# Performance work log

Hardware: AMD Instinct MI355X
Metric: run time of the kernel (lower is better)

Reference implementation:

```python
import jax, jax.numpy as jnp
import numpy as np

KERNEL = 3
PAD = (KERNEL - 1) // 2  # 'same' padding applied manually, conv itself is VALID


def _conv2d(x, w, padding):
    # x: (N,H,W,Cin), w: (kh,kw,Cin,Cout)
    return jax.lax.conv_general_dilated(
        x, w, window_strides=(1, 1), padding=padding,
        dimension_numbers=('NHWC', 'HWIO', 'NHWC'))


def convlstm2d(x, kernel, rec_kernel, bias):
    """Keras ConvLSTM2D (valid input conv on pre-padded input, SAME recurrent conv).

    x: (B,T,H,W,Cin); kernel: (k,k,Cin,4F); rec_kernel: (k,k,F,4F); bias: (4F,)
    Returns full hidden sequence (B,T,H,W,F).
    """
    # tf.pad with paddings [[0,0],[0,0],[p,p],[p,p],[0,0]] (constant mode)
    xp = jnp.pad(x, ((0, 0), (0, 0), (PAD, PAD), (PAD, PAD), (0, 0)))
    B, T = x.shape[:2]
    # Fuse the input-to-hidden conv across all timesteps in one big conv
    xz = _conv2d(xp.reshape((B * T,) + xp.shape[2:]), kernel, 'VALID') + bias
    H, W, F4 = xz.shape[1:]
    F = F4 // 4
    xz = xz.reshape(B, T, H, W, F4).transpose(1, 0, 2, 3, 4)  # (T,B,H,W,4F)

    def step(carry, xt):
        h, c = carry
        z = xt + _conv2d(h, rec_kernel, 'SAME')
        zi, zf, zc, zo = jnp.split(z, 4, axis=-1)  # Keras gate order i,f,c,o
        i = jax.nn.sigmoid(zi)
        f = jax.nn.sigmoid(zf)
        c = f * c + i * jnp.tanh(zc)
        o = jax.nn.sigmoid(zo)
        h = o * jnp.tanh(c)
        return (h, c), h

    h0 = jnp.zeros((B, H, W, F), x.dtype)
    (_, _), hs = jax.lax.scan(step, (h0, h0), xz)
    return hs.transpose(1, 0, 2, 3, 4)  # (B,T,H,W,F)


def setup_inputs() -> dict:
    key = jax.random.key(0)
    ks = jax.random.split(key, 7)
    B, T, H, W, Cin, F = 4, 16, 64, 64, 32, 32
    std = float(np.sqrt(2.0 / (KERNEL * KERNEL * F)))  # he-style kernel init
    x = jax.random.normal(ks[0], (B, T, H, W, Cin), jnp.float32)
    k1 = jax.random.normal(ks[1], (KERNEL, KERNEL, Cin, 4 * F), jnp.float32) * std
    rk1 = jax.random.normal(ks[2], (KERNEL, KERNEL, F, 4 * F), jnp.float32) * std
    b1 = jnp.zeros((4 * F,), jnp.float32)
    k2 = jax.random.normal(ks[3], (KERNEL, KERNEL, F, 4 * F), jnp.float32) * std
    rk2 = jax.random.normal(ks[4], (KERNEL, KERNEL, F, 4 * F), jnp.float32) * std
    b2 = jnp.zeros((4 * F,), jnp.float32)
    return {"x": x, "k1": k1, "rk1": rk1, "b1": b1, "k2": k2, "rk2": rk2, "b2": b2}


def reference(x, k1, rk1, b1, k2, rk2, b2):
    # normalization=None -> identity; pad + ConvLSTM2D, twice
    h = convlstm2d(x, k1, rk1, b1)
    h = convlstm2d(h, k2, rk2, b2)
    return h
```

## Files before the change

kernel.cpp:

```cpp
#include <hip/hip_runtime.h>


typedef __bf16 bf16x8 __attribute__((ext_vector_type(8)));
typedef float f32x4 __attribute__((ext_vector_type(4)));

#define WPK_ELEMS 73728
#define PLANE 524288

__device__ __forceinline__ float fsigmoid(float z) {
    return 1.0f / (1.0f + __expf(-z));
}
__device__ __forceinline__ float ftanh(float z) {
    z = fminf(15.0f, fmaxf(-15.0f, z));
    float e = __expf(2.0f * z);
    return (e - 1.0f) / (e + 1.0f);
}

__global__ __launch_bounds__(256) void pack_weights(
    const float* __restrict__ wk1, const float* __restrict__ wr1,
    const float* __restrict__ wk2, const float* __restrict__ wr2,
    __bf16* __restrict__ wpk)
{
    int i = blockIdx.x * 256 + threadIdx.x;
    if (i >= 2 * WPK_ELEMS) return;
    int layer = i / WPK_ELEMS;
    int r = i - layer * WPK_ELEMS;
    int j2 = r & 7;
    int L  = (r >> 3) & 63;
    int nt = (r >> 9) & 7;
    int cix = r >> 12;
    int tap = cix >> 1, src = cix & 1;
    int s = ((L >> 4) << 3) + j2;
    int gate = nt & 3;
    int f = ((nt >> 2) << 4) + (L & 15);
    int n = (gate << 5) + f;
    const float* w = layer ? (src ? wr2 : wk2) : (src ? wr1 : wk1);
    wpk[i] = (__bf16)w[(tap * 32 + s) * 128 + n];
}

__device__ __forceinline__ bf16x8 cvt8(const float* p) {
    const float4 f0 = *(const float4*)p;
    const float4 f1 = *(const float4*)(p + 4);
    bf16x8 v;
    v[0] = (__bf16)f0.x; v[1] = (__bf16)f0.y;
    v[2] = (__bf16)f0.z; v[3] = (__bf16)f0.w;
    v[4] = (__bf16)f1.x; v[5] = (__bf16)f1.y;
    v[6] = (__bf16)f1.z; v[7] = (__bf16)f1.w;
    return v;
}

#define MFMA8(A0, A1, WP)                                                              \
    acc[0][0] = __builtin_amdgcn_mfma_f32_16x16x32_bf16(A0, WP[0],   acc[0][0], 0, 0, 0); \
    acc[0][1] = __builtin_amdgcn_mfma_f32_16x16x32_bf16(A0, WP[64],  acc[0][1], 0, 0, 0); \
    acc[0][2] = __builtin_amdgcn_mfma_f32_16x16x32_bf16(A0, WP[128], acc[0][2], 0, 0, 0); \
    acc[0][3] = __builtin_amdgcn_mfma_f32_16x16x32_bf16(A0, WP[192], acc[0][3], 0, 0, 0); \
    acc[1][0] = __builtin_amdgcn_mfma_f32_16x16x32_bf16(A1, WP[0],   acc[1][0], 0, 0, 0); \
    acc[1][1] = __builtin_amdgcn_mfma_f32_16x16x32_bf16(A1, WP[64],  acc[1][1], 0, 0, 0); \
    acc[1][2] = __builtin_amdgcn_mfma_f32_16x16x32_bf16(A1, WP[128], acc[1][2], 0, 0, 0); \
    acc[1][3] = __builtin_amdgcn_mfma_f32_16x16x32_bf16(A1, WP[192], acc[1][3], 0, 0, 0);

#define MFMA4(A0, WP)                                                                  \
    acc1[0] = __builtin_amdgcn_mfma_f32_16x16x32_bf16(A0, WP[0],   acc1[0], 0, 0, 0);     \
    acc1[1] = __builtin_amdgcn_mfma_f32_16x16x32_bf16(A0, WP[64],  acc1[1], 0, 0, 0);     \
    acc1[2] = __builtin_amdgcn_mfma_f32_16x16x32_bf16(A0, WP[128], acc1[2], 0, 0, 0);     \
    acc1[3] = __builtin_amdgcn_mfma_f32_16x16x32_bf16(A0, WP[192], acc1[3], 0, 0, 0);

__global__ __launch_bounds__(1024, 1) void clstm_pair3(
    const float* __restrict__ x,
    const __bf16* __restrict__ wpk1, const __bf16* __restrict__ wpk2,
    const float* __restrict__ bias1, const float* __restrict__ bias2,
    __bf16* __restrict__ h1buf,
    __bf16* __restrict__ h2buf,
    float* __restrict__ c1,
    float* __restrict__ c2,
    float* __restrict__ out, int j)
{
    __shared__ __bf16 tXA[6 * 66 * 36];
    __shared__ __bf16 tRA[6 * 66 * 36];
    __shared__ __bf16 tXB[4 * 66 * 36];
    __shared__ __bf16 tHA[4 * 66 * 36];
    __shared__ float  cpass[2 * 64 * 32];

    const int blk = blockIdx.x;
    const int k = blk >> 3;
    const int layer = k >> 4;
    if (layer ? (j < 1) : (j > 7)) return;
    const int grp = (blk & 7) * 16 + (k & 15);
    const int T0 = layer ? (2 * j - 2) : (2 * j);
    const int R = grp << 1;
    const int b = R >> 6, y0 = R & 63;

    const int tid = threadIdx.x;
    const int wid = tid >> 6, L = tid & 63;
    const int c = L & 15, q = L >> 4;

    const int wr  = wid >> 2;
    const int fhA = (wid >> 1) & 1;
    const int mpA = wid & 1;
    const int fA  = fhA * 16 + c;
    const int o   = wid >> 3;
    const int fhB = (wid >> 2) & 1;
    const int pxq = wid & 3;
    const int fB  = fhB * 16 + c;

    const bf16x8* wpkv = (const bf16x8*)(layer ? wpk2 : wpk1);
    const float* bias = layer ? bias2 : bias1;
    float bvA[4], bvB[4];
    #pragma unroll
    for (int g = 0; g < 4; ++g) {
        bvA[g] = bias[g * 32 + fA];
        bvB[g] = bias[g * 32 + fB];
    }

    const float*  xA  = x + (size_t)(b * 16 + T0) * 131072;
    const float*  xB  = xA + 131072;
    const __bf16* h1A = h1buf + (size_t)(T0 & 3) * PLANE;
    const __bf16* h1B = h1buf + (size_t)((T0 + 1) & 3) * PLANE;
    const __bf16* hRA = layer ? (h2buf + (size_t)(((T0 - 1) >> 1) & 1) * PLANE)
                              : (h1buf + (size_t)((T0 - 1) & 3) * PLANE);

    const int n1 = T0 ? 3168 : 1584;
    for (int i = tid; i < n1; i += 1024) {
        const int tile = (i >= 1584);
        const int r2 = i - tile * 1584;
        const int g = r2 & 3;
        const int rc = r2 >> 2;
        const int cc = rc % 66;
        const int row = rc / 66;
        const int yy = y0 - 2 + row;
        const int xc = cc - 1;
        bf16x8 v = {};
        if (yy >= 0 && yy < 64 && xc >= 0 && xc < 64) {
            if (!layer && !tile) {
                v = cvt8(xA + ((size_t)yy * 64 + xc) * 32 + g * 8);
            } else {
                const __bf16* s = tile ? hRA : h1A;
                v = *(const bf16x8*)(s + (((size_t)(b * 64 + yy)) * 64 + xc) * 32 + g * 8);
            }
        }
        *(bf16x8*)((tile ? tRA : tXA) + (row * 66 + cc) * 36 + g * 8) = v;
    }
    for (int i = tid; i < 1056; i += 1024) {
        const int g = i & 3;
        const int rc = i >> 2;
        const int cc = rc % 66;
        const int row = rc / 66;
        const int yy = y0 - 1 + row;
        const int xc = cc - 1;
        bf16x8 v = {};
        if (yy >= 0 && yy < 64 && xc >= 0 && xc < 64) {
            if (!layer) v = cvt8(xB + ((size_t)yy * 64 + xc) * 32 + g * 8);
            else        v = *(const bf16x8*)(h1B + (((size_t)(b * 64 + yy)) * 64 + xc) * 32 + g * 8);
        }
        *(bf16x8*)(tXB + (row * 66 + cc) * 36 + g * 8) = v;
    }
    for (int i = tid; i < 1188; i += 1024)
        *(bf16x8*)(tHA + i * 8) = (bf16x8){};
    __syncthreads();

    {
        const int ra = y0 - 1 + wr;
        const bool rvalid = (ra >= 0 && ra < 64);
        const bool own = (wr == 1 || wr == 2);
        const float* crd = (layer ? c2 : c1) + (size_t)(((T0 - 1) >> 1) & 1) * PLANE;
        const size_t rowA = (size_t)(b * 64 + (rvalid ? ra : 0)) * 2048;

        f32x4 acc[2][4];
        #pragma unroll
        for (int m2 = 0; m2 < 2; ++m2)
            #pragma unroll
            for (int g = 0; g < 4; ++g)
                acc[m2][g] = (f32x4){bvA[g], bvA[g], bvA[g], bvA[g]};

        #pragma unroll
        for (int tap = 0; tap < 9; ++tap) {
            const int dyk = tap / 3, dxk = tap % 3;
            const int lb = ((wr + dyk) * 66 + mpA * 32 + c + dxk) * 36 + q * 8;
            const bf16x8 a0 = *(const bf16x8*)(tXA + lb);
            const bf16x8 a1 = *(const bf16x8*)(tXA + lb + 16 * 36);
            const bf16x8* wpx = wpkv + (size_t)((tap * 2) * 8 + fhA * 4) * 64 + L;
            MFMA8(a0, a1, wpx);
            if (T0 > 0) {
                const bf16x8 h0 = *(const bf16x8*)(tRA + lb);
                const bf16x8 h1v = *(const bf16x8*)(tRA + lb + 16 * 36);
                const bf16x8* wph = wpkv + (size_t)((tap * 2 + 1) * 8 + fhA * 4) * 64 + L;
                MFMA8(h0, h1v, wph);
            }
        }
        #pragma unroll
        for (int m2 = 0; m2 < 2; ++m2) {
            #pragma unroll
            for (int r = 0; r < 4; ++r) {
                const int px = mpA * 32 + m2 * 16 + q * 4 + r;
                const float ig = fsigmoid(acc[m2][0][r]);
                const float fg = fsigmoid(acc[m2][1][r]);
                const float gg = ftanh(acc[m2][2][r]);
                const float og = fsigmoid(acc[m2][3][r]);
                float cold = 0.f;
                if (T0 > 0 && rvalid) cold = crd[rowA + (size_t)px * 32 + fA];
                const float cn = (T0 ? fg * cold : 0.f) + ig * gg;
                const float hv = og * ftanh(cn);
                if (rvalid) tHA[(wr * 66 + px + 1) * 36 + fA] = (__bf16)hv;
                if (own) {
                    cpass[(wr - 1) * 2048 + px * 32 + fA] = cn;
                    if (layer)
                        out[((size_t)(b * 16 + T0) * 4096 + (size_t)ra * 64 + px) * 32 + fA] = hv;
                    else
                        h1buf[(size_t)(T0 & 3) * PLANE + rowA + (size_t)px * 32 + fA] = (__bf16)hv;
                }
            }
        }
    }
    __syncthreads();

    {
        const int rb = y0 + o;
        float* cwr = (layer ? c2 : c1) + (size_t)(((T0 + 1) >> 1) & 1) * PLANE;

        f32x4 acc1[4];
        #pragma unroll
        for (int g = 0; g < 4; ++g)
            acc1[g] = (f32x4){bvB[g], bvB[g], bvB[g], bvB[g]};

        #pragma unroll
        for (int tap = 0; tap < 9; ++tap) {
            const int dyk = tap / 3, dxk = tap % 3;
            const int lb = ((o + dyk) * 66 + pxq * 16 + c + dxk) * 36 + q * 8;
            const bf16x8 a0 = *(const bf16x8*)(tXB + lb);
            const bf16x8* wpx = wpkv + (size_t)((tap * 2) * 8 + fhB * 4) * 64 + L;
            MFMA4(a0, wpx);
            const bf16x8 h0 = *(const bf16x8*)(tHA + lb);
            const bf16x8* wph = wpkv + (size_t)((tap * 2 + 1) * 8 + fhB * 4) * 64 + L;
            MFMA4(h0, wph);
        }
        const size_t rowB = (size_t)(b * 64 + rb) * 2048;
        __bf16* h2w = h2buf + (size_t)(((T0 + 1) >> 1) & 1) * PLANE;
        #pragma unroll
        for (int r = 0; r < 4; ++r) {
            const int px = pxq * 16 + q * 4 + r;
            const float ig = fsigmoid(acc1[0][r]);
            const float fg = fsigmoid(acc1[1][r]);
            const float gg = ftanh(acc1[2][r]);
            const float og = fsigmoid(acc1[3][r]);
            const float cold = cpass[o * 2048 + px * 32 + fB];
            const float cn = fg * cold + ig * gg;
            const float hv = og * ftanh(cn);
            cwr[rowB + (size_t)px * 32 + fB] = cn;
            if (layer) {
                out[((size_t)(b * 16 + T0 + 1) * 4096 + (size_t)rb * 64 + px) * 32 + fB] = hv;
                h2w[rowB + (size_t)px * 32 + fB] = (__bf16)hv;
            } else {
                h1buf[(size_t)((T0 + 1) & 3) * PLANE + rowB + (size_t)px * 32 + fB] = (__bf16)hv;
            }
        }
    }
}

extern "C" void kernel_launch(void* const* d_in, const int* in_sizes, int n_in,
                              void* d_out, int out_size, void* d_ws, size_t ws_size,
                              hipStream_t stream)
{
    const float* x   = (const float*)d_in[0];
    const float* k1  = (const float*)d_in[1];
    const float* rk1 = (const float*)d_in[2];
    const float* b1  = (const float*)d_in[3];
    const float* k2  = (const float*)d_in[4];
    const float* rk2 = (const float*)d_in[5];
    const float* b2  = (const float*)d_in[6];
    float* out = (float*)d_out;

    __bf16* wpk1  = (__bf16*)d_ws;
    __bf16* wpk2  = wpk1 + WPK_ELEMS;
    __bf16* h1buf = wpk2 + WPK_ELEMS;
    __bf16* h2buf = h1buf + 4 * (size_t)PLANE;
    float*  c1    = (float*)(h2buf + 2 * (size_t)PLANE);
    float*  c2    = c1 + 2 * (size_t)PLANE;

    pack_weights<<<(2 * WPK_ELEMS + 255) / 256, 256, 0, stream>>>(k1, rk1, k2, rk2, wpk1);

    for (int j = 0; j <= 8; ++j) {
        clstm_pair3<<<256, 1024, 0, stream>>>(
            x, wpk1, wpk2, b1, b2, h1buf, h2buf, c1, c2, out, j);
    }
}
```

Measured before the change: 260.7 us.

## Widen per-wave M tile to 64 pixels and overlap step-B input conv

Each wave now computes a full 64-pixel row across four M sub-tiles, reusing each loaded weight fragment across 16 MFMAs instead of 8 or 4. Only 12 of the 16 waves do work: 8 handle step A for their row, and 4 compute step B's input-conv part in parallel with step A. After the barrier those 4 finish only the recurrent part. This cuts redundant weight loads and moves work off the critical path, at the cost of more accumulator registers and 4 idle waves per block.

```diff
diff --git a/kernel.cpp b/kernel.cpp
--- a/kernel.cpp
+++ b/kernel.cpp
@@ -49,23 +49,28 @@
     return v;
 }
 
-#define MFMA8(A0, A1, WP)                                                              \
-    acc[0][0] = __builtin_amdgcn_mfma_f32_16x16x32_bf16(A0, WP[0],   acc[0][0], 0, 0, 0); \
-    acc[0][1] = __builtin_amdgcn_mfma_f32_16x16x32_bf16(A0, WP[64],  acc[0][1], 0, 0, 0); \
-    acc[0][2] = __builtin_amdgcn_mfma_f32_16x16x32_bf16(A0, WP[128], acc[0][2], 0, 0, 0); \
-    acc[0][3] = __builtin_amdgcn_mfma_f32_16x16x32_bf16(A0, WP[192], acc[0][3], 0, 0, 0); \
-    acc[1][0] = __builtin_amdgcn_mfma_f32_16x16x32_bf16(A1, WP[0],   acc[1][0], 0, 0, 0); \
-    acc[1][1] = __builtin_amdgcn_mfma_f32_16x16x32_bf16(A1, WP[64],  acc[1][1], 0, 0, 0); \
-    acc[1][2] = __builtin_amdgcn_mfma_f32_16x16x32_bf16(A1, WP[128], acc[1][2], 0, 0, 0); \
-    acc[1][3] = __builtin_amdgcn_mfma_f32_16x16x32_bf16(A1, WP[192], acc[1][3], 0, 0, 0);
-
-#define MFMA4(A0, WP)                                                                  \
-    acc1[0] = __builtin_amdgcn_mfma_f32_16x16x32_bf16(A0, WP[0],   acc1[0], 0, 0, 0);     \
-    acc1[1] = __builtin_amdgcn_mfma_f32_16x16x32_bf16(A0, WP[64],  acc1[1], 0, 0, 0);     \
-    acc1[2] = __builtin_amdgcn_mfma_f32_16x16x32_bf16(A0, WP[128], acc1[2], 0, 0, 0);     \
-    acc1[3] = __builtin_amdgcn_mfma_f32_16x16x32_bf16(A0, WP[192], acc1[3], 0, 0, 0);
-
-__global__ __launch_bounds__(1024, 1) void clstm_pair3(
+#define MFMA16(A0, A1, A2, A3, WP, ACC)                                                   \
+    {                                                                                     \
+        const bf16x8 w0 = WP[0], w1 = WP[64], w2 = WP[128], w3 = WP[192];                 \
+        ACC[0][0] = __builtin_amdgcn_mfma_f32_16x16x32_bf16(A0, w0, ACC[0][0], 0, 0, 0);  \
+        ACC[0][1] = __builtin_amdgcn_mfma_f32_16x16x32_bf16(A0, w1, ACC[0][1], 0, 0, 0);  \
+        ACC[0][2] = __builtin_amdgcn_mfma_f32_16x16x32_bf16(A0, w2, ACC[0][2], 0, 0, 0);  \
+        ACC[0][3] = __builtin_amdgcn_mfma_f32_16x16x32_bf16(A0, w3, ACC[0][3], 0, 0, 0);  \
+        ACC[1][0] = __builtin_amdgcn_mfma_f32_16x16x32_bf16(A1, w0, ACC[1][0], 0, 0, 0);  \
+        ACC[1][1] = __builtin_amdgcn_mfma_f32_16x16x32_bf16(A1, w1, ACC[1][1], 0, 0, 0);  \
+        ACC[1][2] = __builtin_amdgcn_mfma_f32_16x16x32_bf16(A1, w2, ACC[1][2], 0, 0, 0);  \
+        ACC[1][3] = __builtin_amdgcn_mfma_f32_16x16x32_bf16(A1, w3, ACC[1][3], 0, 0, 0);  \
+        ACC[2][0] = __builtin_amdgcn_mfma_f32_16x16x32_bf16(A2, w0, ACC[2][0], 0, 0, 0);  \
+        ACC[2][1] = __builtin_amdgcn_mfma_f32_16x16x32_bf16(A2, w1, ACC[2][1], 0, 0, 0);  \
+        ACC[2][2] = __builtin_amdgcn_mfma_f32_16x16x32_bf16(A2, w2, ACC[2][2], 0, 0, 0);  \
+        ACC[2][3] = __builtin_amdgcn_mfma_f32_16x16x32_bf16(A2, w3, ACC[2][3], 0, 0, 0);  \
+        ACC[3][0] = __builtin_amdgcn_mfma_f32_16x16x32_bf16(A3, w0, ACC[3][0], 0, 0, 0);  \
+        ACC[3][1] = __builtin_amdgcn_mfma_f32_16x16x32_bf16(A3, w1, ACC[3][1], 0, 0, 0);  \
+        ACC[3][2] = __builtin_amdgcn_mfma_f32_16x16x32_bf16(A3, w2, ACC[3][2], 0, 0, 0);  \
+        ACC[3][3] = __builtin_amdgcn_mfma_f32_16x16x32_bf16(A3, w3, ACC[3][3], 0, 0, 0);  \
+    }
+
+__global__ __launch_bounds__(1024, 1) void clstm_m64(
     const float* __restrict__ x,
     const __bf16* __restrict__ wpk1, const __bf16* __restrict__ wpk2,
     const float* __restrict__ bias1, const float* __restrict__ bias2,
@@ -92,25 +97,11 @@
 
     const int tid = threadIdx.x;
     const int wid = tid >> 6, L = tid & 63;
-    const int c = L & 15, q = L >> 4;
-
-    const int wr  = wid >> 2;
-    const int fhA = (wid >> 1) & 1;
-    const int mpA = wid & 1;
-    const int fA  = fhA * 16 + c;
-    const int o   = wid >> 3;
-    const int fhB = (wid >> 2) & 1;
-    const int pxq = wid & 3;
-    const int fB  = fhB * 16 + c;
+    const int c = L & 15, q = L >> 4, q8 = q * 8;
 
     const bf16x8* wpkv = (const bf16x8*)(layer ? wpk2 : wpk1);
     const float* bias = layer ? bias2 : bias1;
-    float bvA[4], bvB[4];
-    #pragma unroll
-    for (int g = 0; g < 4; ++g) {
-        bvA[g] = bias[g * 32 + fA];
-        bvB[g] = bias[g * 32 + fB];
-    }
+    float* cl = layer ? c2 : c1;
 
     const float*  xA  = x + (size_t)(b * 16 + T0) * 131072;
     const float*  xB  = xA + 131072;
@@ -130,7 +121,7 @@
         const int yy = y0 - 2 + row;
         const int xc = cc - 1;
         bf16x8 v = {};
-        if (yy >= 0 && yy < 64 && xc >= 0 && xc < 64) {
+        if ((unsigned)yy < 64u && (unsigned)xc < 64u) {
             if (!layer && !tile) {
                 v = cvt8(xA + ((size_t)yy * 64 + xc) * 32 + g * 8);
             } else {
@@ -148,7 +139,7 @@
         const int yy = y0 - 1 + row;
         const int xc = cc - 1;
         bf16x8 v = {};
-        if (yy >= 0 && yy < 64 && xc >= 0 && xc < 64) {
+        if ((unsigned)yy < 64u && (unsigned)xc < 64u) {
             if (!layer) v = cvt8(xB + ((size_t)yy * 64 + xc) * 32 + g * 8);
             else        v = *(const bf16x8*)(h1B + (((size_t)(b * 64 + yy)) * 64 + xc) * 32 + g * 8);
         }
@@ -158,99 +149,138 @@
         *(bf16x8*)(tHA + i * 8) = (bf16x8){};
     __syncthreads();
 
-    {
+    f32x4 accB[4][4];
+
+    if (wid < 8) {
+        const int wr = wid >> 1, fh = wid & 1;
+        const int f = fh * 16 + c;
         const int ra = y0 - 1 + wr;
-        const bool rvalid = (ra >= 0 && ra < 64);
-        const bool own = (wr == 1 || wr == 2);
-        const float* crd = (layer ? c2 : c1) + (size_t)(((T0 - 1) >> 1) & 1) * PLANE;
-        const size_t rowA = (size_t)(b * 64 + (rvalid ? ra : 0)) * 2048;
-
-        f32x4 acc[2][4];
-        #pragma unroll
-        for (int m2 = 0; m2 < 2; ++m2)
-            #pragma unroll
-            for (int g = 0; g < 4; ++g)
-                acc[m2][g] = (f32x4){bvA[g], bvA[g], bvA[g], bvA[g]};
-
-        #pragma unroll
-        for (int tap = 0; tap < 9; ++tap) {
-            const int dyk = tap / 3, dxk = tap % 3;
-            const int lb = ((wr + dyk) * 66 + mpA * 32 + c + dxk) * 36 + q * 8;
-            const bf16x8 a0 = *(const bf16x8*)(tXA + lb);
-            const bf16x8 a1 = *(const bf16x8*)(tXA + lb + 16 * 36);
-            const bf16x8* wpx = wpkv + (size_t)((tap * 2) * 8 + fhA * 4) * 64 + L;
-            MFMA8(a0, a1, wpx);
-            if (T0 > 0) {
-                const bf16x8 h0 = *(const bf16x8*)(tRA + lb);
-                const bf16x8 h1v = *(const bf16x8*)(tRA + lb + 16 * 36);
-                const bf16x8* wph = wpkv + (size_t)((tap * 2 + 1) * 8 + fhA * 4) * 64 + L;
-                MFMA8(h0, h1v, wph);
-            }
-        }
-        #pragma unroll
-        for (int m2 = 0; m2 < 2; ++m2) {
-            #pragma unroll
-            for (int r = 0; r < 4; ++r) {
-                const int px = mpA * 32 + m2 * 16 + q * 4 + r;
-                const float ig = fsigmoid(acc[m2][0][r]);
-                const float fg = fsigmoid(acc[m2][1][r]);
-                const float gg = ftanh(acc[m2][2][r]);
-                const float og = fsigmoid(acc[m2][3][r]);
-                float cold = 0.f;
-                if (T0 > 0 && rvalid) cold = crd[rowA + (size_t)px * 32 + fA];
-                const float cn = (T0 ? fg * cold : 0.f) + ig * gg;
-                const float hv = og * ftanh(cn);
-                if (rvalid) tHA[(wr * 66 + px + 1) * 36 + fA] = (__bf16)hv;
-                if (own) {
-                    cpass[(wr - 1) * 2048 + px * 32 + fA] = cn;
-                    if (layer)
-                        out[((size_t)(b * 16 + T0) * 4096 + (size_t)ra * 64 + px) * 32 + fA] = hv;
-                    else
-                        h1buf[(size_t)(T0 & 3) * PLANE + rowA + (size_t)px * 32 + fA] = (__bf16)hv;
+        const bool rv = ((unsigned)ra < 64u);
+        if (rv) {
+            float bv[4];
+            #pragma unroll
+            for (int g = 0; g < 4; ++g) bv[g] = bias[g * 32 + f];
+
+            f32x4 acc[4][4];
+            #pragma unroll
+            for (int m = 0; m < 4; ++m)
+                #pragma unroll
+                for (int g = 0; g < 4; ++g)
+                    acc[m][g] = (f32x4){bv[g], bv[g], bv[g], bv[g]};
+
+            #pragma unroll
+            for (int tap = 0; tap < 9; ++tap) {
+                const int dyk = tap / 3, dxk = tap - dyk * 3;
+                const int lb = ((wr + dyk) * 66 + c + dxk) * 36 + q8;
+                {
+                    const bf16x8 a0 = *(const bf16x8*)(tXA + lb);
+                    const bf16x8 a1 = *(const bf16x8*)(tXA + lb + 16 * 36);
+                    const bf16x8 a2 = *(const bf16x8*)(tXA + lb + 32 * 36);
+                    const bf16x8 a3 = *(const bf16x8*)(tXA + lb + 48 * 36);
+                    const bf16x8* wp = wpkv + (size_t)((tap * 2) * 8 + fh * 4) * 64 + L;
+                    MFMA16(a0, a1, a2, a3, wp, acc);
+                }
+                if (T0 > 0) {
+                    const bf16x8 h0 = *(const bf16x8*)(tRA + lb);
+                    const bf16x8 h1v = *(const bf16x8*)(tRA + lb + 16 * 36);
+                    const bf16x8 h2v = *(const bf16x8*)(tRA + lb + 32 * 36);
+                    const bf16x8 h3v = *(const bf16x8*)(tRA + lb + 48 * 36);
+                    const bf16x8* wp = wpkv + (size_t)((tap * 2 + 1) * 8 + fh * 4) * 64 + L;
+                    MFMA16(h0, h1v, h2v, h3v, wp, acc);
                 }
             }
+
+            const bool own = (wr == 1 || wr == 2);
+            const float* crd = cl + (size_t)((j - 1) & 1) * PLANE;
+            const size_t rowA = (size_t)(b * 64 + ra) * 2048;
+            #pragma unroll
+            for (int m = 0; m < 4; ++m) {
+                #pragma unroll
+                for (int r = 0; r < 4; ++r) {
+                    const int px = m * 16 + q * 4 + r;
+                    const float ig = fsigmoid(acc[m][0][r]);
+                    const float fg = fsigmoid(acc[m][1][r]);
+                    const float gg = ftanh(acc[m][2][r]);
+                    const float og = fsigmoid(acc[m][3][r]);
+                    const float cold = T0 ? crd[rowA + (size_t)px * 32 + f] : 0.0f;
+                    const float cn = (T0 ? fg * cold : 0.0f) + ig * gg;
+                    const float hv = og * ftanh(cn);
+                    tHA[(wr * 66 + px + 1) * 36 + f] = (__bf16)hv;
+                    if (own) {
+                        cpass[(wr - 1) * 2048 + px * 32 + f] = cn;
+                        if (layer)
+                            out[((size_t)(b * 16 + T0) * 4096 + (size_t)ra * 64 + px) * 32 + f] = hv;
+                        else
+                            h1buf[(size_t)(T0 & 3) * PLANE + rowA + (size_t)px * 32 + f] = (__bf16)hv;
+                    }
+                }
+            }
+        }
+    } else if (wid < 12) {
+        const int u = wid - 8;
+        const int o = u >> 1, fh = u & 1;
+        const int f = fh * 16 + c;
+        float bv[4];
+        #pragma unroll
+        for (int g = 0; g < 4; ++g) bv[g] = bias[g * 32 + f];
+        #pragma unroll
+        for (int m = 0; m < 4; ++m)
+            #pragma unroll
+            for (int g = 0; g < 4; ++g)
+                accB[m][g] = (f32x4){bv[g], bv[g], bv[g], bv[g]};
+
+        #pragma unroll
+        for (int tap = 0; tap < 9; ++tap) {
+            const int dyk = tap / 3, dxk = tap - dyk * 3;
+            const int lb = ((o + dyk) * 66 + c + dxk) * 36 + q8;
+            const bf16x8 a0 = *(const bf16x8*)(tXB + lb);
+            const bf16x8 a1 = *(const bf16x8*)(tXB + lb + 16 * 36);
+            const bf16x8 a2 = *(const bf16x8*)(tXB + lb + 32 * 36);
+            const bf16x8 a3 = *(const bf16x8*)(tXB + lb + 48 * 36);
+            const bf16x8* wp = wpkv + (size_t)((tap * 2) * 8 + fh * 4) * 64 + L;
+            MFMA16(a0, a1, a2, a3, wp, accB);
         }
     }
     __syncthreads();
 
-    {
+    if (wid >= 8 && wid < 12) {
+        const int u = wid - 8;
+        const int o = u >> 1, fh = u & 1;
+        const int f = fh * 16 + c;
+        #pragma unroll
+        for (int tap = 0; tap < 9; ++tap) {
+            const int dyk = tap / 3, dxk = tap - dyk * 3;
+            const int lb = ((o + dyk) * 66 + c + dxk) * 36 + q8;
+            const bf16x8 h0 = *(const bf16x8*)(tHA + lb);
+            const bf16x8 h1v = *(const bf16x8*)(tHA + lb + 16 * 36);
+            const bf16x8 h2v = *(const bf16x8*)(tHA + lb + 32 * 36);
+            const bf16x8 h3v = *(const bf16x8*)(tHA + lb + 48 * 36);
+            const bf16x8* wp = wpkv + (size_t)((tap * 2 + 1) * 8 + fh * 4) * 64 + L;
+            MFMA16(h0, h1v, h2v, h3v, wp, accB);
+        }
         const int rb = y0 + o;
-        float* cwr = (layer ? c2 : c1) + (size_t)(((T0 + 1) >> 1) & 1) * PLANE;
-
-        f32x4 acc1[4];
-        #pragma unroll
-        for (int g = 0; g < 4; ++g)
-            acc1[g] = (f32x4){bvB[g], bvB[g], bvB[g], bvB[g]};
-
-        #pragma unroll
-        for (int tap = 0; tap < 9; ++tap) {
-            const int dyk = tap / 3, dxk = tap % 3;
-            const int lb = ((o + dyk) * 66 + pxq * 16 + c + dxk) * 36 + q * 8;
-            const bf16x8 a0 = *(const bf16x8*)(tXB + lb);
-            const bf16x8* wpx = wpkv + (size_t)((tap * 2) * 8 + fhB * 4) * 64 + L;
-            MFMA4(a0, wpx);
-            const bf16x8 h0 = *(const bf16x8*)(tHA + lb);
-            const bf16x8* wph = wpkv + (size_t)((tap * 2 + 1) * 8 + fhB * 4) * 64 + L;
-            MFMA4(h0, wph);
-        }
+        float* cwr = cl + (size_t)(j & 1) * PLANE;
+        __bf16* h2w = h2buf + (size_t)(((T0 + 1) >> 1) & 1) * PLANE;
         const size_t rowB = (size_t)(b * 64 + rb) * 2048;
-        __bf16* h2w = h2buf + (size_t)(((T0 + 1) >> 1) & 1) * PLANE;
-        #pragma unroll
-        for (int r = 0; r < 4; ++r) {
-            const int px = pxq * 16 + q * 4 + r;
-            const float ig = fsigmoid(acc1[0][r]);
-            const float fg = fsigmoid(acc1[1][r]);
-            const float gg = ftanh(acc1[2][r]);
-            const float og = fsigmoid(acc1[3][r]);
-            const float cold = cpass[o * 2048 + px * 32 + fB];
-            const float cn = fg * cold + ig * gg;
-            const float hv = og * ftanh(cn);
-            cwr[rowB + (size_t)px * 32 + fB] = cn;
-            if (layer) {
-                out[((size_t)(b * 16 + T0 + 1) * 4096 + (size_t)rb * 64 + px) * 32 + fB] = hv;
-                h2w[rowB + (size_t)px * 32 + fB] = (__bf16)hv;
-            } else {
-                h1buf[(size_t)((T0 + 1) & 3) * PLANE + rowB + (size_t)px * 32 + fB] = (__bf16)hv;
+        #pragma unroll
+        for (int m = 0; m < 4; ++m) {
+            #pragma unroll
+            for (int r = 0; r < 4; ++r) {
+                const int px = m * 16 + q * 4 + r;
+                const float ig = fsigmoid(accB[m][0][r]);
+                const float fg = fsigmoid(accB[m][1][r]);
+                const float gg = ftanh(accB[m][2][r]);
+                const float og = fsigmoid(accB[m][3][r]);
+                const float cold = cpass[o * 2048 + px * 32 + f];
+                const float cn = fg * cold + ig * gg;
+                const float hv = og * ftanh(cn);
+                cwr[rowB + (size_t)px * 32 + f] = cn;
+                if (layer) {
+                    out[((size_t)(b * 16 + T0 + 1) * 4096 + (size_t)rb * 64 + px) * 32 + f] = hv;
+                    h2w[rowB + (size_t)px * 32 + f] = (__bf16)hv;
+                } else {
+                    h1buf[(size_t)((T0 + 1) & 3) * PLANE + rowB + (size_t)px * 32 + f] = (__bf16)hv;
+                }
             }
         }
     }
@@ -279,7 +309,7 @@
     pack_weights<<<(2 * WPK_ELEMS + 255) / 256, 256, 0, stream>>>(k1, rk1, k2, rk2, wpk1);
 
     for (int j = 0; j <= 8; ++j) {
-        clstm_pair3<<<256, 1024, 0, stream>>>(
+        clstm_m64<<<256, 1024, 0, stream>>>(
             x, wpk1, wpk2, b1, b2, h1buf, h2buf, c1, c2, out, j);
     }
 }
```

Measured after the change: 245.3 us. 1.06x faster.
